# Kernel tuning notes

Hardware: AMD Instinct MI355X
Metric: run time of the kernel (lower is better)

The kernel has to match this reference:

```python
import jax, jax.numpy as jnp
import numpy as np
from jax import lax

N, D, K, R, T = 200000, 128, 64, 4, 50000
L = 2 * R  # positive + negative relation layers
ITERATIONS = 2


def _l2norm(x, eps=1e-12):
    # torch F.normalize(p=2): x / max(||x||, eps)
    n = jnp.sqrt(jnp.sum(x * x, axis=-1, keepdims=True))
    return x / jnp.maximum(n, eps)


def setup_inputs() -> dict:
    key = jax.random.key(0)
    ks = jax.random.split(key, 8)
    # Unique write targets (a permutation) so the last-write scatter is deterministic;
    # matches input_specs' randint intent (indices uniform in [0, N)).
    perm = jax.random.permutation(ks[0], N)
    subj_idx = perm[:T].astype(jnp.int32)
    obj_idx = perm[T:2 * T].astype(jnp.int32)
    layer_idx = jax.random.randint(ks[1], (T,), 0, L, dtype=jnp.int32)
    memberships = jax.random.randint(ks[2], (N, K), 0, 2, dtype=jnp.int32)
    embedding_m = jax.random.normal(ks[3], (N, D), dtype=jnp.float32)
    # ClassUpdate params: [d+K] -> d
    Wc = jax.random.normal(ks[4], (D + K, D), dtype=jnp.float32) / np.sqrt(D + K)
    bc = jnp.zeros((D,), dtype=jnp.float32)
    # RelationUpdate params, one layer per (relation, polarity): [2d] -> [2d]
    Wr = jax.random.normal(ks[5], (L, 2 * D, 2 * D), dtype=jnp.float32) / np.sqrt(2 * D)
    br = jnp.zeros((L, 2 * D), dtype=jnp.float32)
    return {
        'embedding_m': embedding_m,
        'memberships': memberships,
        'subj_idx': subj_idx,
        'obj_idx': obj_idx,
        'layer_idx': layer_idx,
        'Wc': Wc, 'bc': bc, 'Wr': Wr, 'br': br,
    }


def reference(embedding_m, memberships, subj_idx, obj_idx, layer_idx, Wc, bc, Wr, br):
    mem = memberships.astype(embedding_m.dtype)  # [N, K]
    t_ar = jnp.arange(T)

    def iteration(e, _):
        # --- ClassUpdate: e' = l2norm(tanh([e; m] Wc + bc)) ---
        x = jnp.concatenate([e, mem], axis=1)           # [N, d+K]
        e = _l2norm(jnp.tanh(x @ Wc + bc))              # [N, d]
        # --- RelationUpdates: reads come from the post-class-update snapshot `e`
        pair = jnp.concatenate([e[subj_idx], e[obj_idx]], axis=1)   # [T, 2d]
        # compute through all L relation layers, then select each triple's layer
        out_all = jnp.einsum('tc,lcd->tld', pair, Wr) + br          # [T, L, 2d]
        out = jnp.tanh(out_all[t_ar, layer_idx])                    # [T, 2d]
        new_s = _l2norm(out[:, :D])
        new_o = _l2norm(out[:, D:])
        e_next = e.at[subj_idx].set(new_s).at[obj_idx].set(new_o)
        return e_next, None

    e_final, _ = lax.scan(iteration, embedding_m, None, length=ITERATIONS)
    return e_final
```

## Files before the change

kernel.cpp:

```cpp
#include <hip/hip_runtime.h>
#include <hip/hip_bf16.h>


#define NROWS 200000
#define DD    128
#define KK    64
#define TT    50000
#define LL    8
#define BT    64
#define PADT  50560

#define NB    100
#define CHB   500
#define PL    8
#define PREPB 268

#define WS_OFFS   0
#define WS_CNT    64
#define WS_BASE   4096
#define WS_BINS   8192
#define WS_WCP    210432
#define WS_WRP    (WS_WCP + 6*8*64*16)
#define WS_MB     (WS_WRP + 8*8*16*64*16)
#define WS_E16    (WS_MB + NROWS*8)
#define WS_NEED   (WS_E16 + (size_t)NROWS*DD*2)

typedef unsigned short u16;
typedef unsigned int   u32;
typedef unsigned long long u64;
typedef unsigned char  u8;
typedef __attribute__((ext_vector_type(8))) short bf16x8;
typedef __attribute__((ext_vector_type(4))) float f32x4;

#define SWZ(row, byte) ((byte) ^ (((row)&7)<<4))

__device__ __forceinline__ u32 bfbits(float f){
  __hip_bfloat16 h = __float2bfloat16(f);
  return (u32)*reinterpret_cast<unsigned short*>(&h);
}
__device__ __forceinline__ u32 pk(float lo, float hi){
  return bfbits(lo) | (bfbits(hi) << 16);
}
__device__ __forceinline__ float qreduce16(float ss){
  ss += __shfl_xor(ss, 1, 64);
  ss += __shfl_xor(ss, 2, 64);
  ss += __shfl_xor(ss, 4, 64);
  ss += __shfl_xor(ss, 8, 64);
  return ss;
}

__global__ __launch_bounds__(256) void k_prep(
    const float* __restrict__ Wc, const float* __restrict__ Wr,
    uint4* __restrict__ wcp, uint4* __restrict__ wrp,
    const int* __restrict__ layer, int* __restrict__ cnt)
{
  if (blockIdx.x >= PREPB){
    const int bb = blockIdx.x - PREPB, lane = threadIdx.x;
    if (lane >= 64) return;
    const int lim = bb*CHB + CHB;
    int i0 = bb*CHB + lane*PL, i1 = i0 + PL; if (i1 > lim) i1 = lim;
    int c[LL] = {0,0,0,0,0,0,0,0};
    for (int i = i0; i < i1; ++i){
      int l = layer[i];
      #pragma unroll
      for (int k = 0; k < LL; ++k) c[k] += (l == k);
    }
    #pragma unroll
    for (int k = 0; k < LL; ++k){
      int v = c[k];
      v += __shfl_xor(v, 1, 64); v += __shfl_xor(v, 2, 64);
      v += __shfl_xor(v, 4, 64); v += __shfl_xor(v, 8, 64);
      v += __shfl_xor(v, 16, 64); v += __shfl_xor(v, 32, 64);
      if (lane == k) cnt[bb*LL + k] = v;
    }
    return;
  }
  int id = blockIdx.x*blockDim.x + threadIdx.x;
  if (id < 3072){
    int lane = id & 63, nt = (id >> 6) & 7, kt = id >> 9;
    int k0 = kt*32 + (lane>>4)*8, n = nt*16 + (lane&15);
    u32 p[4];
    #pragma unroll
    for (int e2 = 0; e2 < 4; ++e2)
      p[e2] = pk(Wc[(k0 + 2*e2)*DD + n], Wc[(k0 + 2*e2 + 1)*DD + n]);
    wcp[id] = make_uint4(p[0], p[1], p[2], p[3]);
  } else if (id < 3072 + 65536){
    int id2 = id - 3072;
    int lane = id2 & 63, nt = (id2>>6) & 15, kt = (id2>>10) & 7, l = id2 >> 13;
    int k0 = kt*32 + (lane>>4)*8, n = nt*16 + (lane&15);
    const float* w = Wr + (size_t)l*65536;
    u32 p[4];
    #pragma unroll
    for (int e2 = 0; e2 < 4; ++e2)
      p[e2] = pk(w[(k0 + 2*e2)*256 + n], w[(k0 + 2*e2 + 1)*256 + n]);
    wrp[id2] = make_uint4(p[0], p[1], p[2], p[3]);
  }
}

__global__ __launch_bounds__(64) void k_bin2(const int* __restrict__ cnt,
                                             int* __restrict__ offs,
                                             int* __restrict__ gbase,
                                             int* __restrict__ bins)
{
  __shared__ int pre[NB][LL];
  __shared__ int tot[LL], soffs[LL+1];
  const int t = threadIdx.x;
  if (t < LL){
    int acc = 0;
    for (int bb = 0; bb < NB; ++bb){ pre[bb][t] = acc; acc += cnt[bb*LL + t]; }
    tot[t] = acc;
  }
  __syncthreads();
  if (t == 0){
    int acc = 0;
    for (int l = 0; l < LL; ++l){
      soffs[l] = acc; offs[l] = acc;
      acc += ((tot[l] + BT - 1)/BT)*BT;
    }
    soffs[LL] = acc; offs[LL] = acc;
  }
  __syncthreads();
  for (int idx = t; idx < NB*LL; idx += 64){
    int bb = idx >> 3, k = idx & 7;
    gbase[idx] = soffs[k] + pre[bb][k];
  }
  const int k = t >> 3, sub = t & 7;
  const int sz = soffs[k+1] - soffs[k];
  for (int i = tot[k] + sub; i < sz; i += 8) bins[soffs[k] + i] = -1;
}

__global__ __launch_bounds__(64) void k_bin3(const int* __restrict__ layer,
                                             const int* __restrict__ gbase,
                                             int* __restrict__ bins)
{
  const int bb = blockIdx.x, lane = threadIdx.x;
  const int lim = bb*CHB + CHB;
  int i0 = bb*CHB + lane*PL, i1 = i0 + PL; if (i1 > lim) i1 = lim;
  int c[LL] = {0,0,0,0,0,0,0,0};
  for (int i = i0; i < i1; ++i){
    int l = layer[i];
    #pragma unroll
    for (int k = 0; k < LL; ++k) c[k] += (l == k);
  }
  int start[LL];
  #pragma unroll
  for (int k = 0; k < LL; ++k){
    int v = c[k];
    #pragma unroll
    for (int d = 1; d < 64; d <<= 1){
      int u = __shfl_up(v, d, 64);
      if (lane >= d) v += u;
    }
    start[k] = gbase[bb*LL + k] + v - c[k];
  }
  for (int i = i0; i < i1; ++i){
    int l = layer[i];
    #pragma unroll
    for (int k = 0; k < LL; ++k)
      if (l == k) bins[start[k]++] = i;
  }
}

template<bool S16, bool MBITS, bool W16, bool WF32>
__global__ __launch_bounds__(256) void k_class(
    const float* __restrict__ srcf, const u16* __restrict__ src16,
    u16* __restrict__ e16, float* __restrict__ dstf,
    const int* __restrict__ mem, u64* __restrict__ mbits,
    const uint4* __restrict__ wcp, const float* __restrict__ bc)
{
  __shared__ u16   sW[6*8*64*8];
  __shared__ u16   sA[64*192];
  __shared__ float sBc[DD];

  const int tid = threadIdx.x;
  {
    uint4* sw = (uint4*)sW;
    for (int i = tid; i < 3072; i += 256) sw[i] = wcp[i];
    if (tid < DD) sBc[tid] = bc[tid];
  }
  const int lane = tid & 63, wid = tid >> 6;
  const int colj = lane & 15, qw = lane >> 4;

  for (int rb = blockIdx.x; rb < NROWS/64; rb += gridDim.x){
    const int rowbase = rb * 64;
    __syncthreads();
    #pragma unroll
    for (int v = 0; v < 4; ++v){
      int f = (v*256 + tid) * 8;
      int row = f >> 7, col = f & 127;
      uint4 out;
      if constexpr (S16){
        out = *(const uint4*)(src16 + (size_t)(rowbase+row)*DD + col);
      } else {
        const float4* s4 = (const float4*)(srcf + (size_t)(rowbase+row)*DD + col);
        float4 a = s4[0], b = s4[1];
        out = make_uint4(pk(a.x,a.y), pk(a.z,a.w), pk(b.x,b.y), pk(b.z,b.w));
      }
      *(uint4*)((char*)sA + row*384 + SWZ(row, col*2)) = out;
    }
    if constexpr (MBITS){
      const int r = tid >> 2, q = tid & 3;
      u64 m = mbits[rowbase + r];
      u32 s = (u32)(m >> (q*16)) & 0xFFFFu;
      u32 p[8];
      #pragma unroll
      for (int jj = 0; jj < 8; ++jj){
        u32 lo = (s >> (2*jj))     & 1u;
        u32 hi = (s >> (2*jj + 1)) & 1u;
        p[jj] = (lo ? 0x3F80u : 0u) | (hi ? 0x3F800000u : 0u);
      }
      *(uint4*)((char*)sA + r*384 + SWZ(r, 256 + q*32))      = make_uint4(p[0],p[1],p[2],p[3]);
      *(uint4*)((char*)sA + r*384 + SWZ(r, 256 + q*32 + 16)) = make_uint4(p[4],p[5],p[6],p[7]);
    } else {
      u8* mb8 = (u8*)mbits;
      #pragma unroll
      for (int v = 0; v < 2; ++v){
        int f = (v*256 + tid) * 8;
        int row = f >> 6, col = f & 63;
        const int4* s4 = (const int4*)(mem + (size_t)(rowbase+row)*KK + col);
        int4 a = s4[0], b = s4[1];
        u32 p0 = (a.x?0x3F80u:0u) | ((a.y?0x3F80u:0u)<<16);
        u32 p1 = (a.z?0x3F80u:0u) | ((a.w?0x3F80u:0u)<<16);
        u32 p2 = (b.x?0x3F80u:0u) | ((b.y?0x3F80u:0u)<<16);
        u32 p3 = (b.z?0x3F80u:0u) | ((b.w?0x3F80u:0u)<<16);
        *(uint4*)((char*)sA + row*384 + SWZ(row, 256 + col*2)) =
          make_uint4(p0, p1, p2, p3);
        u8 byte = (u8)((a.x!=0) | ((a.y!=0)<<1) | ((a.z!=0)<<2) | ((a.w!=0)<<3)
                 | ((b.x!=0)<<4) | ((b.y!=0)<<5) | ((b.z!=0)<<6) | ((b.w!=0)<<7));
        mb8[(size_t)(rowbase+row)*8 + (col>>3)] = byte;
      }
    }
    __syncthreads();

    bf16x8 afr[6];
    #pragma unroll
    for (int kt = 0; kt < 6; ++kt){
      int row = wid*16 + colj;
      afr[kt] = *(bf16x8*)((char*)sA + row*384 + SWZ(row, kt*64 + qw*16));
    }
    f32x4 acc[8];
    #pragma unroll
    for (int nt = 0; nt < 8; ++nt) acc[nt] = (f32x4){0.f,0.f,0.f,0.f};
    #pragma unroll
    for (int nt = 0; nt < 8; ++nt){
      #pragma unroll
      for (int kt = 0; kt < 6; ++kt){
        bf16x8 bfr = *(bf16x8*)&sW[((kt*8 + nt)*64 + lane)*8];
        acc[nt] = __builtin_amdgcn_mfma_f32_16x16x32_bf16(afr[kt], bfr, acc[nt], 0,0,0);
      }
    }
    #pragma unroll
    for (int r = 0; r < 4; ++r){
      int grow = rowbase + wid*16 + qw*4 + r;
      float t[8], ss = 0.f;
      #pragma unroll
      for (int nt = 0; nt < 8; ++nt){
        t[nt] = tanhf(acc[nt][r] + sBc[nt*16 + colj]);
        ss += t[nt]*t[nt];
      }
      ss = qreduce16(ss);
      float sc = 1.0f / fmaxf(sqrtf(ss), 1e-12f);
      #pragma unroll
      for (int nt = 0; nt < 8; ++nt){
        float v = t[nt]*sc;
        if constexpr (W16)
          e16[(size_t)grow*DD + nt*16 + colj] = (u16)bfbits(v);
        if constexpr (WF32)
          dstf[(size_t)grow*DD + nt*16 + colj] = v;
      }
    }
  }
}

template<bool S16, bool W16, bool WF32>
__global__ __launch_bounds__(256) void k_rel(
    const float* __restrict__ ef32, u16* __restrict__ e16,
    float* __restrict__ dstf,
    const int* __restrict__ subj, const int* __restrict__ obj,
    const uint4* __restrict__ wrp, const float* __restrict__ br,
    const int* __restrict__ offs, const int* __restrict__ bins)
{
  __shared__ u16   sA[64*256];
  __shared__ float sBr[256];
  __shared__ float sPart[BT][4];
  __shared__ int   sS[BT], sO[BT];

  const int tid  = threadIdx.x;
  const int base = blockIdx.x * BT;
  if (base >= offs[LL]) return;
  int l = 0;
  while (l < LL-1 && base >= offs[l+1]) ++l;

  const int lane = tid & 63, wid = tid >> 6;
  const int colj = lane & 15, qw = lane >> 4;

  const uint4* wb = wrp + (size_t)l*8192 + lane;
  bf16x8 wf[8][4];
  #pragma unroll
  for (int n = 0; n < 4; ++n){
    wf[0][n] = *(const bf16x8*)&wb[(0*16 + wid*4 + n)*64];
    wf[1][n] = *(const bf16x8*)&wb[(1*16 + wid*4 + n)*64];
  }

  sBr[tid] = br[l*256 + tid];

  const int ti = tid >> 2, q = tid & 3;
  int id = bins[base + ti];
  int rs = -1, ro = -1;
  if (id >= 0){ rs = subj[id]; ro = obj[id]; }
  if (q == 0){ sS[ti] = rs; sO[ti] = ro; }
  const int rr = (q < 2) ? rs : ro;
  if constexpr (S16){
    const u16* srcp = e16 + (size_t)rr*DD + (q & 1)*64;
    #pragma unroll
    for (int j = 0; j < 8; ++j){
      uint4 w = (id >= 0) ? ((const uint4*)srcp)[j] : make_uint4(0u,0u,0u,0u);
      *(uint4*)((char*)sA + ti*512 + SWZ(ti, q*128 + j*16)) = w;
    }
  } else {
    const float* srcp = ef32 + (size_t)rr*DD + (q & 1)*64;
    #pragma unroll
    for (int j = 0; j < 8; ++j){
      uint4 w;
      if (id >= 0){
        float4 a = ((const float4*)srcp)[2*j], b = ((const float4*)srcp)[2*j+1];
        w = make_uint4(pk(a.x,a.y), pk(a.z,a.w), pk(b.x,b.y), pk(b.z,b.w));
      } else w = make_uint4(0u,0u,0u,0u);
      *(uint4*)((char*)sA + ti*512 + SWZ(ti, q*128 + j*16)) = w;
    }
  }
  __syncthreads();

  f32x4 acc[4][4];
  #pragma unroll
  for (int m = 0; m < 4; ++m)
    #pragma unroll
    for (int n = 0; n < 4; ++n) acc[m][n] = (f32x4){0.f,0.f,0.f,0.f};

  #pragma unroll
  for (int kt = 0; kt < 8; ++kt){
    if (kt + 2 < 8){
      #pragma unroll
      for (int n = 0; n < 4; ++n)
        wf[kt+2][n] = *(const bf16x8*)&wb[((kt+2)*16 + wid*4 + n)*64];
    }
    #pragma unroll
    for (int m = 0; m < 4; ++m){
      int row = m*16 + colj;
      bf16x8 afr = *(bf16x8*)((char*)sA + row*512 + SWZ(row, kt*64 + qw*16));
      #pragma unroll
      for (int n = 0; n < 4; ++n)
        acc[m][n] = __builtin_amdgcn_mfma_f32_16x16x32_bf16(afr, wf[kt][n], acc[m][n], 0,0,0);
    }
  }

  #pragma unroll
  for (int m = 0; m < 4; ++m){
    #pragma unroll
    for (int n = 0; n < 4; ++n){
      float b = sBr[(wid*4 + n)*16 + colj];
      #pragma unroll
      for (int r = 0; r < 4; ++r)
        acc[m][n][r] = tanhf(acc[m][n][r] + b);
    }
    #pragma unroll
    for (int r = 0; r < 4; ++r){
      float ss = acc[m][0][r]*acc[m][0][r] + acc[m][1][r]*acc[m][1][r]
               + acc[m][2][r]*acc[m][2][r] + acc[m][3][r]*acc[m][3][r];
      ss = qreduce16(ss);
      if (colj == 0) sPart[m*16 + qw*4 + r][wid] = ss;
    }
  }
  __syncthreads();

  const int h = wid >> 1;
  #pragma unroll
  for (int m = 0; m < 4; ++m){
    #pragma unroll
    for (int r = 0; r < 4; ++r){
      int tri = m*16 + qw*4 + r;
      int row = h ? sO[tri] : sS[tri];
      if (row < 0) continue;
      float ss = sPart[tri][2*h] + sPart[tri][2*h + 1];
      float sc = 1.0f / fmaxf(sqrtf(ss), 1e-12f);
      #pragma unroll
      for (int n = 0; n < 4; ++n){
        int cc = (wid*4 + n)*16 + colj - h*DD;
        float v = acc[m][n][r]*sc;
        if constexpr (W16)
          e16[(size_t)row*DD + cc] = (u16)bfbits(v);
        if constexpr (WF32)
          dstf[(size_t)row*DD + cc] = v;
      }
    }
  }
}

extern "C" void kernel_launch(void* const* d_in, const int* in_sizes, int n_in,
                              void* d_out, int out_size, void* d_ws, size_t ws_size,
                              hipStream_t stream) {
  (void)in_sizes; (void)n_in; (void)out_size;
  const float* emb  = (const float*)d_in[0];
  const int*   mem  = (const int*)  d_in[1];
  const int*   subj = (const int*)  d_in[2];
  const int*   obj  = (const int*)  d_in[3];
  const int*   lay  = (const int*)  d_in[4];
  const float* Wc   = (const float*)d_in[5];
  const float* bc   = (const float*)d_in[6];
  const float* Wr   = (const float*)d_in[7];
  const float* br   = (const float*)d_in[8];

  float* e   = (float*)d_out;
  char*  wsb = (char*)d_ws;
  int*   offs  = (int*)(wsb + WS_OFFS);
  int*   cnt   = (int*)(wsb + WS_CNT);
  int*   gbase = (int*)(wsb + WS_BASE);
  int*   bins  = (int*)(wsb + WS_BINS);
  uint4* wcp   = (uint4*)(wsb + WS_WCP);
  uint4* wrp   = (uint4*)(wsb + WS_WRP);
  u64*   mbits = (u64*)(wsb + WS_MB);
  u16*   e16   = (u16*)(wsb + WS_E16);

  k_prep<<<PREPB + NB, 256, 0, stream>>>(Wc, Wr, wcp, wrp, lay, cnt);
  k_bin2<<<1, 64, 0, stream>>>(cnt, offs, gbase, bins);
  k_bin3<<<NB, 64, 0, stream>>>(lay, gbase, bins);

  if (ws_size >= WS_NEED){
    k_class<false,false,true,false><<<512, 256, 0, stream>>>(
        emb, nullptr, e16, nullptr, mem, mbits, wcp, bc);
    k_rel<true,true,false><<<PADT/BT, 256, 0, stream>>>(
        nullptr, e16, nullptr, subj, obj, wrp, br, offs, bins);
    k_class<true,true,false,true><<<512, 256, 0, stream>>>(
        nullptr, e16, nullptr, e, mem, mbits, wcp, bc);
    k_rel<false,false,true><<<PADT/BT, 256, 0, stream>>>(
        e, nullptr, e, subj, obj, wrp, br, offs, bins);
  } else {
    k_class<false,false,false,true><<<512, 256, 0, stream>>>(
        emb, nullptr, nullptr, e, mem, mbits, wcp, bc);
    k_rel<false,false,true><<<PADT/BT, 256, 0, stream>>>(
        e, nullptr, e, subj, obj, wrp, br, offs, bins);
    k_class<false,true,false,true><<<512, 256, 0, stream>>>(
        e, nullptr, nullptr, e, mem, mbits, wcp, bc);
    k_rel<false,false,true><<<PADT/BT, 256, 0, stream>>>(
        e, nullptr, e, subj, obj, wrp, br, offs, bins);
  }
}
```

Baseline: 204.8 us.

## Keep class-update weights in registers, split columns across waves, use fast tanh

The class-update kernel no longer stages the full Wc fragment set in shared memory. Each wave now holds in registers the weight fragments for its own two 16-column tiles and computes all 64 rows, and the per-row norm is combined across waves through a small shared-memory partial-sum buffer and an extra barrier. Both kernels replace tanhf and the exact sqrt/divide with an exp-based fast tanh and hardware rcp/sqrt approximations, and the class grid is doubled to 1024 blocks. The aim is to cut LDS traffic and transcendental cost and raise occupancy, at the price of slightly lower numerical accuracy and an extra sync per row block.

```diff
diff --git a/kernel.cpp b/kernel.cpp
--- a/kernel.cpp
+++ b/kernel.cpp
@@ -47,6 +47,15 @@
   ss += __shfl_xor(ss, 4, 64);
   ss += __shfl_xor(ss, 8, 64);
   return ss;
+}
+__device__ __forceinline__ float fast_tanh(float x){
+  float a = fabsf(x);
+  float e = __expf(-2.0f*a);
+  float t = (1.0f - e) * __builtin_amdgcn_rcpf(1.0f + e);
+  return copysignf(t, x);
+}
+__device__ __forceinline__ float rnorm_scale(float ss){
+  return __builtin_amdgcn_rcpf(fmaxf(__builtin_amdgcn_sqrtf(ss), 1e-12f));
 }
 
 __global__ __launch_bounds__(256) void k_prep(
@@ -168,18 +177,25 @@
     const int* __restrict__ mem, u64* __restrict__ mbits,
     const uint4* __restrict__ wcp, const float* __restrict__ bc)
 {
-  __shared__ u16   sW[6*8*64*8];
   __shared__ u16   sA[64*192];
   __shared__ float sBc[DD];
+  __shared__ float sPart[64][4];
 
   const int tid = threadIdx.x;
-  {
-    uint4* sw = (uint4*)sW;
-    for (int i = tid; i < 3072; i += 256) sw[i] = wcp[i];
-    if (tid < DD) sBc[tid] = bc[tid];
-  }
   const int lane = tid & 63, wid = tid >> 6;
   const int colj = lane & 15, qw = lane >> 4;
+
+  bf16x8 wf[6][2];
+  #pragma unroll
+  for (int kt = 0; kt < 6; ++kt)
+    #pragma unroll
+    for (int j = 0; j < 2; ++j)
+      wf[kt][j] = *(const bf16x8*)&wcp[(kt*8 + 2*wid + j)*64 + lane];
+  if (tid < DD) sBc[tid] = bc[tid];
+
+  const float b0 = bc[(2*wid)*16 + colj];
+  const float b1 = bc[(2*wid+1)*16 + colj];
+  (void)sBc;
 
   for (int rb = blockIdx.x; rb < NROWS/64; rb += gridDim.x){
     const int rowbase = rb * 64;
@@ -232,41 +248,52 @@
     }
     __syncthreads();
 
-    bf16x8 afr[6];
-    #pragma unroll
-    for (int kt = 0; kt < 6; ++kt){
-      int row = wid*16 + colj;
-      afr[kt] = *(bf16x8*)((char*)sA + row*384 + SWZ(row, kt*64 + qw*16));
-    }
-    f32x4 acc[8];
-    #pragma unroll
-    for (int nt = 0; nt < 8; ++nt) acc[nt] = (f32x4){0.f,0.f,0.f,0.f};
-    #pragma unroll
-    for (int nt = 0; nt < 8; ++nt){
+    f32x4 acc[4][2];
+    #pragma unroll
+    for (int m = 0; m < 4; ++m){
+      acc[m][0] = (f32x4){0.f,0.f,0.f,0.f};
+      acc[m][1] = (f32x4){0.f,0.f,0.f,0.f};
+    }
+    #pragma unroll
+    for (int m = 0; m < 4; ++m){
+      int row = m*16 + colj;
       #pragma unroll
       for (int kt = 0; kt < 6; ++kt){
-        bf16x8 bfr = *(bf16x8*)&sW[((kt*8 + nt)*64 + lane)*8];
-        acc[nt] = __builtin_amdgcn_mfma_f32_16x16x32_bf16(afr[kt], bfr, acc[nt], 0,0,0);
-      }
-    }
-    #pragma unroll
-    for (int r = 0; r < 4; ++r){
-      int grow = rowbase + wid*16 + qw*4 + r;
-      float t[8], ss = 0.f;
-      #pragma unroll
-      for (int nt = 0; nt < 8; ++nt){
-        t[nt] = tanhf(acc[nt][r] + sBc[nt*16 + colj]);
-        ss += t[nt]*t[nt];
-      }
-      ss = qreduce16(ss);
-      float sc = 1.0f / fmaxf(sqrtf(ss), 1e-12f);
-      #pragma unroll
-      for (int nt = 0; nt < 8; ++nt){
-        float v = t[nt]*sc;
-        if constexpr (W16)
-          e16[(size_t)grow*DD + nt*16 + colj] = (u16)bfbits(v);
-        if constexpr (WF32)
-          dstf[(size_t)grow*DD + nt*16 + colj] = v;
+        bf16x8 afr = *(bf16x8*)((char*)sA + row*384 + SWZ(row, kt*64 + qw*16));
+        acc[m][0] = __builtin_amdgcn_mfma_f32_16x16x32_bf16(afr, wf[kt][0], acc[m][0], 0,0,0);
+        acc[m][1] = __builtin_amdgcn_mfma_f32_16x16x32_bf16(afr, wf[kt][1], acc[m][1], 0,0,0);
+      }
+    }
+    #pragma unroll
+    for (int m = 0; m < 4; ++m){
+      #pragma unroll
+      for (int r = 0; r < 4; ++r){
+        float t0 = fast_tanh(acc[m][0][r] + b0);
+        float t1 = fast_tanh(acc[m][1][r] + b1);
+        acc[m][0][r] = t0; acc[m][1][r] = t1;
+        float ss = qreduce16(t0*t0 + t1*t1);
+        if (colj == 0) sPart[m*16 + qw*4 + r][wid] = ss;
+      }
+    }
+    __syncthreads();
+    #pragma unroll
+    for (int m = 0; m < 4; ++m){
+      #pragma unroll
+      for (int r = 0; r < 4; ++r){
+        int tri = m*16 + qw*4 + r;
+        f32x4 p = *(f32x4*)sPart[tri];
+        float sc = rnorm_scale(p[0] + p[1] + p[2] + p[3]);
+        int grow = rowbase + tri;
+        float v0 = acc[m][0][r]*sc, v1 = acc[m][1][r]*sc;
+        int c0 = (2*wid)*16 + colj;
+        if constexpr (W16){
+          e16[(size_t)grow*DD + c0]      = (u16)bfbits(v0);
+          e16[(size_t)grow*DD + c0 + 16] = (u16)bfbits(v1);
+        }
+        if constexpr (WF32){
+          dstf[(size_t)grow*DD + c0]      = v0;
+          dstf[(size_t)grow*DD + c0 + 16] = v1;
+        }
       }
     }
   }
@@ -361,7 +388,7 @@
       float b = sBr[(wid*4 + n)*16 + colj];
       #pragma unroll
       for (int r = 0; r < 4; ++r)
-        acc[m][n][r] = tanhf(acc[m][n][r] + b);
+        acc[m][n][r] = fast_tanh(acc[m][n][r] + b);
     }
     #pragma unroll
     for (int r = 0; r < 4; ++r){
@@ -382,7 +409,7 @@
       int row = h ? sO[tri] : sS[tri];
       if (row < 0) continue;
       float ss = sPart[tri][2*h] + sPart[tri][2*h + 1];
-      float sc = 1.0f / fmaxf(sqrtf(ss), 1e-12f);
+      float sc = rnorm_scale(ss);
       #pragma unroll
       for (int n = 0; n < 4; ++n){
         int cc = (wid*4 + n)*16 + colj - h*DD;
@@ -426,20 +453,20 @@
   k_bin3<<<NB, 64, 0, stream>>>(lay, gbase, bins);
 
   if (ws_size >= WS_NEED){
-    k_class<false,false,true,false><<<512, 256, 0, stream>>>(
+    k_class<false,false,true,false><<<1024, 256, 0, stream>>>(
         emb, nullptr, e16, nullptr, mem, mbits, wcp, bc);
     k_rel<true,true,false><<<PADT/BT, 256, 0, stream>>>(
         nullptr, e16, nullptr, subj, obj, wrp, br, offs, bins);
-    k_class<true,true,false,true><<<512, 256, 0, stream>>>(
+    k_class<true,true,false,true><<<1024, 256, 0, stream>>>(
         nullptr, e16, nullptr, e, mem, mbits, wcp, bc);
     k_rel<false,false,true><<<PADT/BT, 256, 0, stream>>>(
         e, nullptr, e, subj, obj, wrp, br, offs, bins);
   } else {
-    k_class<false,false,false,true><<<512, 256, 0, stream>>>(
+    k_class<false,false,false,true><<<1024, 256, 0, stream>>>(
         emb, nullptr, nullptr, e, mem, mbits, wcp, bc);
     k_rel<false,false,true><<<PADT/BT, 256, 0, stream>>>(
         e, nullptr, e, subj, obj, wrp, br, offs, bins);
-    k_class<false,true,false,true><<<512, 256, 0, stream>>>(
+    k_class<false,true,false,true><<<1024, 256, 0, stream>>>(
         e, nullptr, nullptr, e, mem, mbits, wcp, bc);
     k_rel<false,false,true><<<PADT/BT, 256, 0, stream>>>(
         e, nullptr, e, subj, obj, wrp, br, offs, bins);
```

Result: faster. 184.2 us (-10.1%).
